# Kernel tuning notes

Hardware: AMD Instinct MI355X
Metric: run time of the kernel (lower is better)

The kernel has to match this reference:

```python
import jax, jax.numpy as jnp
import numpy as np
import math

NHEADS = 16
CAUSAL = True
NEG_INF = -1e18


def setup_inputs() -> dict:
    key = jax.random.key(0)
    kq, kk, kv = jax.random.split(key, 3)
    B, S, D = 4, 8192, 1024
    q = jax.random.normal(kq, (B, S, D), dtype=jnp.float32)
    k = jax.random.normal(kk, (B, S, D), dtype=jnp.float32)
    v = jax.random.normal(kv, (B, S, D), dtype=jnp.float32)
    return {"q": q, "k": k, "v": v}


def reference(q, k, v):
    # Faithful to the torch code: it views (B,S,H*hd)->(B,S,H,hd) WITHOUT
    # transposing heads to dim 1, so matmul(q, k^T) is an (H,H) score matrix
    # per token -- attention across HEADS, causal mask/softmax over heads.
    B, S, D = q.shape
    hd = D // NHEADS
    qh = q.reshape(B, S, NHEADS, hd)
    kh = k.reshape(B, S, NHEADS, hd)
    vh = v.reshape(B, S, NHEADS, hd)
    # scores: (B, S, H, H)
    scores = jnp.einsum('bsqd,bskd->bsqk', qh, kh) / math.sqrt(hd)
    if CAUSAL:
        mask = jnp.tril(jnp.ones((NHEADS, NHEADS), dtype=bool))
        scores = jnp.where(mask, scores, jnp.asarray(NEG_INF, scores.dtype))
    attn = jax.nn.softmax(scores, axis=-1)
    out = jnp.einsum('bsqk,bskd->bsqd', attn, vh)
    return out.reshape(B, S, D)
```

## Files before the change

### kernel.cpp

```cpp
#include <hip/hip_runtime.h>
#include <math.h>

#define NHEADS 16
#define HD 64
#define DMODEL 1024
#define QK_PAD 68

__global__ __launch_bounds__(256) void temporal_attn_kernel(
    const float* __restrict__ q,
    const float* __restrict__ k,
    const float* __restrict__ v,
    float* __restrict__ out)
{
    __shared__ float  qs[NHEADS * QK_PAD];
    __shared__ float  ks[NHEADS * QK_PAD];
    __shared__ float4 vs[NHEADS * (HD / 4)];
    __shared__ float  ps[NHEADS][NHEADS + 1];

    const int t = threadIdx.x;
    const size_t base = (size_t)blockIdx.x * DMODEL;
    const int r = t >> 4;
    const int c = t & 15;

    const float4 qv = ((const float4*)(q + base))[t];
    const float4 kv = ((const float4*)(k + base))[t];
    const float4 vv = ((const float4*)(v + base))[t];
    *((float4*)&qs[r * QK_PAD + 4 * c]) = qv;
    *((float4*)&ks[r * QK_PAD + 4 * c]) = kv;
    vs[t] = vv;
    __syncthreads();

    const float4* qi = (const float4*)&qs[r * QK_PAD];
    const float4* kj = (const float4*)&ks[c * QK_PAD];
    float acc = 0.f;
    #pragma unroll
    for (int d = 0; d < HD / 4; ++d) {
        const float4 a = qi[d];
        const float4 b = kj[d];
        acc = fmaf(a.x, b.x, acc);
        acc = fmaf(a.y, b.y, acc);
        acc = fmaf(a.z, b.z, acc);
        acc = fmaf(a.w, b.w, acc);
    }
    acc *= 0.125f;
    if (c > r) acc = -1e30f;

    float m = acc;
    #pragma unroll
    for (int mask = 8; mask >= 1; mask >>= 1)
        m = fmaxf(m, __shfl_xor(m, mask, 16));
    const float p = __expf(acc - m);
    float s = p;
    #pragma unroll
    for (int mask = 8; mask >= 1; mask >>= 1)
        s += __shfl_xor(s, mask, 16);
    ps[r][c] = p / s;
    __syncthreads();

    float4 o = make_float4(0.f, 0.f, 0.f, 0.f);
    #pragma unroll
    for (int j = 0; j < NHEADS; ++j) {
        const float  pij = ps[r][j];
        const float4 vj  = vs[j * (HD / 4) + c];
        o.x = fmaf(pij, vj.x, o.x);
        o.y = fmaf(pij, vj.y, o.y);
        o.z = fmaf(pij, vj.z, o.z);
        o.w = fmaf(pij, vj.w, o.w);
    }
    ((float4*)(out + base))[t] = o;
}

extern "C" void kernel_launch(void* const* d_in, const int* in_sizes, int n_in,
                              void* d_out, int out_size, void* d_ws, size_t ws_size,
                              hipStream_t stream) {
    const float* q = (const float*)d_in[0];
    const float* k = (const float*)d_in[1];
    const float* v = (const float*)d_in[2];
    float* o = (float*)d_out;
    const int ntok = in_sizes[0] / DMODEL;
    temporal_attn_kernel<<<ntok, 256, 0, stream>>>(q, k, v, o);
}
```

Measured before the change: 96.78 us.

## Compute per-token head attention with fp16 MFMA, one token per wavefront

Replaces the shared-memory FP32 kernel with one that assigns each wavefront one token (four tokens per block). Q·K^T and P·V run as fp16 MFMA instructions on register-resident operands, and the shared memory and both block barriers are removed. The kernel is memory-bound (about 400MB moved), so the main intended win is less LDS traffic and synchronisation. In exchange, inputs are rounded to fp16, which lowers accuracy, and the V loads and output stores become scalar strided accesses that may coalesce worse.

```diff
diff --git a/kernel.cpp b/kernel.cpp
--- a/kernel.cpp
+++ b/kernel.cpp
@@ -1,10 +1,12 @@
 #include <hip/hip_runtime.h>
 #include <math.h>
 
-#define NHEADS 16
-#define HD 64
 #define DMODEL 1024
-#define QK_PAD 68
+#define TOKW 4
+
+typedef _Float16 f16x4 __attribute__((ext_vector_type(4)));
+typedef _Float16 f16x8 __attribute__((ext_vector_type(8)));
+typedef float    f32x4 __attribute__((ext_vector_type(4)));
 
 __global__ __launch_bounds__(256) void temporal_attn_kernel(
     const float* __restrict__ q,
@@ -12,62 +14,79 @@
     const float* __restrict__ v,
     float* __restrict__ out)
 {
-    __shared__ float  qs[NHEADS * QK_PAD];
-    __shared__ float  ks[NHEADS * QK_PAD];
-    __shared__ float4 vs[NHEADS * (HD / 4)];
-    __shared__ float  ps[NHEADS][NHEADS + 1];
+    const int lane = threadIdx.x & 63;
+    const int wave = threadIdx.x >> 6;
+    const int r = lane & 15;
+    const int G = lane >> 4;
+    const size_t base = ((size_t)blockIdx.x * TOKW + wave) * DMODEL;
 
-    const int t = threadIdx.x;
-    const size_t base = (size_t)blockIdx.x * DMODEL;
-    const int r = t >> 4;
-    const int c = t & 15;
+    const float* qrow = q + base + r * 64;
+    const float* krow = k + base + r * 64;
+    f32x4 ql[4], kl[4];
+#pragma unroll
+    for (int c = 0; c < 2; ++c)
+#pragma unroll
+        for (int h = 0; h < 2; ++h) {
+            ql[2 * c + h] = *(const f32x4*)(qrow + 32 * c + 8 * G + 4 * h);
+            kl[2 * c + h] = *(const f32x4*)(krow + 32 * c + 8 * G + 4 * h);
+        }
+    float vl[4][4];
+#pragma unroll
+    for (int t = 0; t < 4; ++t)
+#pragma unroll
+        for (int cg = 0; cg < 4; ++cg)
+            vl[t][cg] = v[base + (size_t)(4 * G + t) * 64 + 16 * cg + r];
 
-    const float4 qv = ((const float4*)(q + base))[t];
-    const float4 kv = ((const float4*)(k + base))[t];
-    const float4 vv = ((const float4*)(v + base))[t];
-    *((float4*)&qs[r * QK_PAD + 4 * c]) = qv;
-    *((float4*)&ks[r * QK_PAD + 4 * c]) = kv;
-    vs[t] = vv;
-    __syncthreads();
+    f16x8 ka[2], qb[2];
+#pragma unroll
+    for (int c = 0; c < 2; ++c)
+#pragma unroll
+        for (int h = 0; h < 2; ++h)
+#pragma unroll
+            for (int e = 0; e < 4; ++e) {
+                ka[c][4 * h + e] = (_Float16)kl[2 * c + h][e];
+                qb[c][4 * h + e] = (_Float16)ql[2 * c + h][e];
+            }
 
-    const float4* qi = (const float4*)&qs[r * QK_PAD];
-    const float4* kj = (const float4*)&ks[c * QK_PAD];
-    float acc = 0.f;
-    #pragma unroll
-    for (int d = 0; d < HD / 4; ++d) {
-        const float4 a = qi[d];
-        const float4 b = kj[d];
-        acc = fmaf(a.x, b.x, acc);
-        acc = fmaf(a.y, b.y, acc);
-        acc = fmaf(a.z, b.z, acc);
-        acc = fmaf(a.w, b.w, acc);
+    f32x4 acc = {0.f, 0.f, 0.f, 0.f};
+    acc = __builtin_amdgcn_mfma_f32_16x16x32_f16(ka[0], qb[0], acc, 0, 0, 0);
+    acc = __builtin_amdgcn_mfma_f32_16x16x32_f16(ka[1], qb[1], acc, 0, 0, 0);
+
+    float s[4];
+#pragma unroll
+    for (int e = 0; e < 4; ++e) {
+        const int j = 4 * G + e;
+        s[e] = (j > r) ? -1e30f : acc[e] * 0.125f;
     }
-    acc *= 0.125f;
-    if (c > r) acc = -1e30f;
+    float m = fmaxf(fmaxf(s[0], s[1]), fmaxf(s[2], s[3]));
+    m = fmaxf(m, __shfl_xor(m, 16));
+    m = fmaxf(m, __shfl_xor(m, 32));
+    const float e0 = __expf(s[0] - m);
+    const float e1 = __expf(s[1] - m);
+    const float e2 = __expf(s[2] - m);
+    const float e3 = __expf(s[3] - m);
+    float sum = e0 + e1 + e2 + e3;
+    sum += __shfl_xor(sum, 16);
+    sum += __shfl_xor(sum, 32);
+    const float inv = 1.0f / sum;
+    f16x4 pa;
+    pa[0] = (_Float16)(e0 * inv);
+    pa[1] = (_Float16)(e1 * inv);
+    pa[2] = (_Float16)(e2 * inv);
+    pa[3] = (_Float16)(e3 * inv);
 
-    float m = acc;
-    #pragma unroll
-    for (int mask = 8; mask >= 1; mask >>= 1)
-        m = fmaxf(m, __shfl_xor(m, mask, 16));
-    const float p = __expf(acc - m);
-    float s = p;
-    #pragma unroll
-    for (int mask = 8; mask >= 1; mask >>= 1)
-        s += __shfl_xor(s, mask, 16);
-    ps[r][c] = p / s;
-    __syncthreads();
-
-    float4 o = make_float4(0.f, 0.f, 0.f, 0.f);
-    #pragma unroll
-    for (int j = 0; j < NHEADS; ++j) {
-        const float  pij = ps[r][j];
-        const float4 vj  = vs[j * (HD / 4) + c];
-        o.x = fmaf(pij, vj.x, o.x);
-        o.y = fmaf(pij, vj.y, o.y);
-        o.z = fmaf(pij, vj.z, o.z);
-        o.w = fmaf(pij, vj.w, o.w);
+#pragma unroll
+    for (int cg = 0; cg < 4; ++cg) {
+        f16x4 vb;
+#pragma unroll
+        for (int t = 0; t < 4; ++t) vb[t] = (_Float16)vl[t][cg];
+        f32x4 o = {0.f, 0.f, 0.f, 0.f};
+        o = __builtin_amdgcn_mfma_f32_16x16x16f16(pa, vb, o, 0, 0, 0);
+        float* obase = out + base + (size_t)(4 * G) * 64 + 16 * cg + r;
+#pragma unroll
+        for (int e = 0; e < 4; ++e)
+            obase[e * 64] = o[e];
     }
-    ((float4*)(out + base))[t] = o;
 }
 
 extern "C" void kernel_launch(void* const* d_in, const int* in_sizes, int n_in,
@@ -78,5 +97,5 @@
     const float* v = (const float*)d_in[2];
     float* o = (float*)d_out;
     const int ntok = in_sizes[0] / DMODEL;
-    temporal_attn_kernel<<<ntok, 256, 0, stream>>>(q, k, v, o);
+    temporal_attn_kernel<<<ntok / TOKW, 256, 0, stream>>>(q, k, v, o);
 }
```

Measured after the change: 96.89 us. About the same (+0.1%).
